# Kernel tuning notes

Hardware: AMD Instinct MI355X
Metric: run time of the kernel (lower is better)

The kernel has to match this reference:

```python
import jax, jax.numpy as jnp
import numpy as np

EPS = 1e-8


def _laplace_normalize(edge_row, edge_col, edge_vals, num_nodes):
    # D_r^{-1/2} A D_c^{-1/2} as in laplace_transform
    deg_r = jax.ops.segment_sum(edge_vals, edge_row, num_segments=num_nodes)
    deg_c = jax.ops.segment_sum(edge_vals, edge_col, num_segments=num_nodes)
    inv_r = 1.0 / (jnp.sqrt(deg_r) + EPS)
    inv_c = 1.0 / (jnp.sqrt(deg_c) + EPS)
    return edge_vals * inv_r[edge_row] * inv_c[edge_col]


def _l2norm(x):
    # F.normalize(p=2, dim=1): x / max(||x||, eps) with eps=1e-12
    n = jnp.sqrt(jnp.sum(x * x, axis=1, keepdims=True))
    return x / jnp.maximum(n, 1e-12)


def setup_inputs() -> dict:
    key = jax.random.key(0)
    k1, k2, k3, k4, k5, k6 = jax.random.split(key, 6)
    N, D, E, B = 100000, 64, 3200000, 4096
    node_features = jax.random.normal(k1, (N, D), dtype=jnp.float32)
    edge_row = jax.random.randint(k2, (E,), 0, N, dtype=jnp.int32)
    edge_col = jax.random.randint(k3, (E,), 0, N, dtype=jnp.int32)
    edge_vals = jnp.ones((E,), dtype=jnp.float32)
    a_id = jax.random.randint(k4, (B,), 0, N, dtype=jnp.int32)
    pos_id = jax.random.randint(k5, (B,), 0, N, dtype=jnp.int32)
    neg_id = jax.random.randint(k6, (B,), 0, N, dtype=jnp.int32)
    return {"node_features": node_features, "edge_row": edge_row,
            "edge_col": edge_col, "edge_vals": edge_vals,
            "a_id": a_id, "pos_id": pos_id, "neg_id": neg_id}


def reference(node_features, edge_row, edge_col, edge_vals, a_id, pos_id, neg_id):
    num_nodes = node_features.shape[0]
    num_layers = 3
    norm_vals = _laplace_normalize(edge_row, edge_col, edge_vals, num_nodes)

    # one_propagate: repeated spmm + per-layer L2 normalize, mean over layers
    features = node_features
    acc = node_features  # layer-0 term of the running sum (not normalized)
    for _ in range(num_layers):
        msgs = norm_vals[:, None] * features[edge_col]  # [E, D]
        features = jax.ops.segment_sum(msgs, edge_row, num_segments=num_nodes)
        acc = acc + _l2norm(features)
    node_rep = acc / (num_layers + 1)

    # BPR loss over batch
    a = node_rep[a_id]
    pos_pred = jnp.sum(a * node_rep[pos_id], axis=1)
    neg_pred = jnp.sum(a * node_rep[neg_id], axis=1)
    loss = jnp.mean(-jax.nn.log_sigmoid(pos_pred - neg_pred))
    return loss
```

## Files before the change

kernel.cpp:

```cpp
#include <hip/hip_runtime.h>
#include <math.h>

#define DDIM 64
#define BUCKET 1024
#define LRSHIFT 17
#define CMASK 0x1FFFF
#define LRMASK 0x3FF
#define NBLK 512
#define TPB_BIN 1024
#define NWV 16
#define TPB_CP 512
#define MAXNB 128

typedef unsigned long long ull;
typedef _Float16 half2_t __attribute__((ext_vector_type(2)));

__device__ inline unsigned int bf16_hi(float v) {
    unsigned int a = __float_as_uint(v);
    return (a + 0x7fffu + ((a >> 16) & 1u)) & 0xffff0000u;
}

__device__ inline unsigned int pk_f16x2(float lo, float hi) {
    return __builtin_bit_cast(unsigned int, __builtin_amdgcn_cvt_pkrtz(lo, hi));
}

__device__ inline half2_t dup_lo16(unsigned int s) {
    return __builtin_bit_cast(half2_t, __builtin_amdgcn_perm(0u, s, 0x01000100u));
}

__device__ inline half2_t h2_shfl_xor(half2_t v, int off) {
    return __builtin_bit_cast(half2_t, __shfl_xor(__builtin_bit_cast(unsigned int, v), off));
}

__global__ void init_fill_kernel(int* __restrict__ gfill_r, int* __restrict__ gfill_c,
                                 int NB, int cap) {
    int k = blockIdx.x * blockDim.x + threadIdx.x;
    if (k < NB) {
        gfill_r[k * 16] = k * cap;
        gfill_c[k * 16] = k * cap;
    }
}

__global__ __launch_bounds__(TPB_BIN)
void binning_kernel(const int* __restrict__ erow, const int* __restrict__ ecol,
                    const float* __restrict__ evals,
                    int* __restrict__ gfill_r, int* __restrict__ gfill_c,
                    ull* __restrict__ br, unsigned int* __restrict__ bc,
                    int E, int NB, int chunk) {
    __shared__ int hr[NWV][MAXNB];
    __shared__ int hc[NWV][MAXNB];
    __shared__ int fr[MAXNB];
    __shared__ int fc[MAXNB];
    int t = threadIdx.x;
    int wv = t >> 6;
    for (int k = t; k < NWV * MAXNB; k += TPB_BIN) { (&hr[0][0])[k] = 0; (&hc[0][0])[k] = 0; }
    __syncthreads();
    int lo = blockIdx.x * chunk;
    int hi = min(E, lo + chunk);
    int nq = (hi - lo) >> 2;
    int rem = (hi - lo) & 3;
    int p0 = t, p1 = t + TPB_BIN;
    bool h0 = p0 < nq, h1 = p1 < nq;
    int4 r40, c40, r41, c41;
    float4 v40, v41;
    if (h0) {
        int i = lo + 4 * p0;
        r40 = *(const int4*)(erow + i);
        c40 = *(const int4*)(ecol + i);
        v40 = *(const float4*)(evals + i);
        atomicAdd(&hr[wv][r40.x >> 10], 1);
        atomicAdd(&hr[wv][r40.y >> 10], 1);
        atomicAdd(&hr[wv][r40.z >> 10], 1);
        atomicAdd(&hr[wv][r40.w >> 10], 1);
        atomicAdd(&hc[wv][c40.x >> 10], 1);
        atomicAdd(&hc[wv][c40.y >> 10], 1);
        atomicAdd(&hc[wv][c40.z >> 10], 1);
        atomicAdd(&hc[wv][c40.w >> 10], 1);
    }
    if (h1) {
        int i = lo + 4 * p1;
        r41 = *(const int4*)(erow + i);
        c41 = *(const int4*)(ecol + i);
        v41 = *(const float4*)(evals + i);
        atomicAdd(&hr[wv][r41.x >> 10], 1);
        atomicAdd(&hr[wv][r41.y >> 10], 1);
        atomicAdd(&hr[wv][r41.z >> 10], 1);
        atomicAdd(&hr[wv][r41.w >> 10], 1);
        atomicAdd(&hc[wv][c41.x >> 10], 1);
        atomicAdd(&hc[wv][c41.y >> 10], 1);
        atomicAdd(&hc[wv][c41.z >> 10], 1);
        atomicAdd(&hc[wv][c41.w >> 10], 1);
    }
    if (t == 0) {
        for (int i = hi - rem; i < hi; i++) {
            atomicAdd(&hr[0][erow[i] >> 10], 1);
            atomicAdd(&hc[0][ecol[i] >> 10], 1);
        }
    }
    __syncthreads();
    if (t < NB) {
        int sr = 0, sc = 0;
        #pragma unroll
        for (int w2 = 0; w2 < NWV; w2++) { sr += hr[w2][t]; sc += hc[w2][t]; }
        fr[t] = atomicAdd(&gfill_r[t * 16], sr);
        fc[t] = atomicAdd(&gfill_c[t * 16], sc);
    }
    __syncthreads();
    if (h0) {
        int pos0 = atomicAdd(&fr[r40.x >> 10], 1);
        int pos1 = atomicAdd(&fr[r40.y >> 10], 1);
        int pos2 = atomicAdd(&fr[r40.z >> 10], 1);
        int pos3 = atomicAdd(&fr[r40.w >> 10], 1);
        br[pos0] = ((ull)__float_as_uint(v40.x) << 32) | ((ull)(r40.x & 1023) << LRSHIFT) | (unsigned)c40.x;
        br[pos1] = ((ull)__float_as_uint(v40.y) << 32) | ((ull)(r40.y & 1023) << LRSHIFT) | (unsigned)c40.y;
        br[pos2] = ((ull)__float_as_uint(v40.z) << 32) | ((ull)(r40.z & 1023) << LRSHIFT) | (unsigned)c40.z;
        br[pos3] = ((ull)__float_as_uint(v40.w) << 32) | ((ull)(r40.w & 1023) << LRSHIFT) | (unsigned)c40.w;
        int q0 = atomicAdd(&fc[c40.x >> 10], 1);
        int q1 = atomicAdd(&fc[c40.y >> 10], 1);
        int q2 = atomicAdd(&fc[c40.z >> 10], 1);
        int q3 = atomicAdd(&fc[c40.w >> 10], 1);
        bc[q0] = bf16_hi(v40.x) | (unsigned)(c40.x & 1023);
        bc[q1] = bf16_hi(v40.y) | (unsigned)(c40.y & 1023);
        bc[q2] = bf16_hi(v40.z) | (unsigned)(c40.z & 1023);
        bc[q3] = bf16_hi(v40.w) | (unsigned)(c40.w & 1023);
    }
    if (h1) {
        int pos0 = atomicAdd(&fr[r41.x >> 10], 1);
        int pos1 = atomicAdd(&fr[r41.y >> 10], 1);
        int pos2 = atomicAdd(&fr[r41.z >> 10], 1);
        int pos3 = atomicAdd(&fr[r41.w >> 10], 1);
        br[pos0] = ((ull)__float_as_uint(v41.x) << 32) | ((ull)(r41.x & 1023) << LRSHIFT) | (unsigned)c41.x;
        br[pos1] = ((ull)__float_as_uint(v41.y) << 32) | ((ull)(r41.y & 1023) << LRSHIFT) | (unsigned)c41.y;
        br[pos2] = ((ull)__float_as_uint(v41.z) << 32) | ((ull)(r41.z & 1023) << LRSHIFT) | (unsigned)c41.z;
        br[pos3] = ((ull)__float_as_uint(v41.w) << 32) | ((ull)(r41.w & 1023) << LRSHIFT) | (unsigned)c41.w;
        int q0 = atomicAdd(&fc[c41.x >> 10], 1);
        int q1 = atomicAdd(&fc[c41.y >> 10], 1);
        int q2 = atomicAdd(&fc[c41.z >> 10], 1);
        int q3 = atomicAdd(&fc[c41.w >> 10], 1);
        bc[q0] = bf16_hi(v41.x) | (unsigned)(c41.x & 1023);
        bc[q1] = bf16_hi(v41.y) | (unsigned)(c41.y & 1023);
        bc[q2] = bf16_hi(v41.z) | (unsigned)(c41.z & 1023);
        bc[q3] = bf16_hi(v41.w) | (unsigned)(c41.w & 1023);
    }
    if (t == 0) {
        for (int i = hi - rem; i < hi; i++) {
            int r = erow[i], c = ecol[i];
            float v = evals[i];
            int pos = atomicAdd(&fr[r >> 10], 1);
            br[pos] = ((ull)__float_as_uint(v) << 32) | ((ull)(r & 1023) << LRSHIFT) | (unsigned)c;
            int pos2 = atomicAdd(&fc[c >> 10], 1);
            bc[pos2] = bf16_hi(v) | (unsigned)(c & 1023);
        }
    }
}

__global__ __launch_bounds__(TPB_CP)
void count_kernel(const ull* __restrict__ br, const unsigned int* __restrict__ bc,
                  const int* __restrict__ gfill_r, const int* __restrict__ gfill_c,
                  int* __restrict__ subcnt, float* __restrict__ subds,
                  float* __restrict__ subdsc, int cap) {
    __shared__ int cnt[BUCKET];
    __shared__ float ds[BUCKET];
    __shared__ float dsc[BUCKET];
    int b = blockIdx.x >> 3, ch = blockIdx.x & 7;
    int t = threadIdx.x;
    for (int k = t; k < BUCKET; k += TPB_CP) { cnt[k] = 0; ds[k] = 0.0f; dsc[k] = 0.0f; }
    __syncthreads();
    int s = b * cap;
    int e = gfill_r[b * 16];
    int len = ((((e - s) + 7) >> 3) + 3) & ~3;
    int cs = s + ch * len, ce = min(e, cs + len);
    int m = cs + ((ce - cs) & ~3);
    for (int i = cs + 4 * t; i < m; i += 4 * TPB_CP) {
        ull p0 = br[i];
        ull p1 = br[i + 1];
        ull p2 = br[i + 2];
        ull p3 = br[i + 3];
        int lr0 = (int)((p0 >> LRSHIFT) & LRMASK);
        int lr1 = (int)((p1 >> LRSHIFT) & LRMASK);
        int lr2 = (int)((p2 >> LRSHIFT) & LRMASK);
        int lr3 = (int)((p3 >> LRSHIFT) & LRMASK);
        atomicAdd(&cnt[lr0], 1);
        atomicAdd(&cnt[lr1], 1);
        atomicAdd(&cnt[lr2], 1);
        atomicAdd(&cnt[lr3], 1);
        atomicAdd(&ds[lr0], __uint_as_float((unsigned)(p0 >> 32)));
        atomicAdd(&ds[lr1], __uint_as_float((unsigned)(p1 >> 32)));
        atomicAdd(&ds[lr2], __uint_as_float((unsigned)(p2 >> 32)));
        atomicAdd(&ds[lr3], __uint_as_float((unsigned)(p3 >> 32)));
    }
    if (t == 0) {
        for (int i = m; i < ce; i++) {
            ull p = br[i];
            int lr = (int)((p >> LRSHIFT) & LRMASK);
            atomicAdd(&cnt[lr], 1);
            atomicAdd(&ds[lr], __uint_as_float((unsigned)(p >> 32)));
        }
    }
    int e2 = gfill_c[b * 16];
    int len2 = ((((e2 - s) + 7) >> 3) + 3) & ~3;
    int cs2 = s + ch * len2, ce2 = min(e2, cs2 + len2);
    int m2 = cs2 + ((ce2 - cs2) & ~3);
    for (int i = cs2 + 4 * t; i < m2; i += 4 * TPB_CP) {
        uint4 p = *(const uint4*)(bc + i);
        atomicAdd(&dsc[p.x & 0x3FFu], __uint_as_float(p.x & 0xffff0000u));
        atomicAdd(&dsc[p.y & 0x3FFu], __uint_as_float(p.y & 0xffff0000u));
        atomicAdd(&dsc[p.z & 0x3FFu], __uint_as_float(p.z & 0xffff0000u));
        atomicAdd(&dsc[p.w & 0x3FFu], __uint_as_float(p.w & 0xffff0000u));
    }
    if (t == 0) {
        for (int i = m2; i < ce2; i++) {
            unsigned int p = bc[i];
            atomicAdd(&dsc[p & 0x3FFu], __uint_as_float(p & 0xffff0000u));
        }
    }
    __syncthreads();
    size_t base = ((size_t)b * 8 + ch) * BUCKET;
    for (int k = t; k < BUCKET; k += TPB_CP) {
        subcnt[base + k] = cnt[k];
        subds[base + k]  = ds[k];
        subdsc[base + k] = dsc[k];
    }
}

__global__ __launch_bounds__(1024)
void combine_kernel(int* __restrict__ subcnt, const float* __restrict__ subds,
                    const float* __restrict__ subdsc,
                    int2* __restrict__ rse,
                    float* __restrict__ inv_r, float* __restrict__ inv_c,
                    int N, int cap) {
    __shared__ int tot[BUCKET];
    int b = blockIdx.x, t = threadIdx.x;
    size_t base = (size_t)b * 8 * BUCKET;
    int c8[8];
    int sum = 0;
    #pragma unroll
    for (int c = 0; c < 8; c++) { c8[c] = subcnt[base + c * BUCKET + t]; sum += c8[c]; }
    int sum2 = (sum + 3) & ~3;
    tot[t] = sum2;
    __syncthreads();
    for (int off = 1; off < BUCKET; off <<= 1) {
        int v = (t >= off) ? tot[t - off] : 0;
        __syncthreads();
        tot[t] += v;
        __syncthreads();
    }
    int excl = tot[t] - sum2;
    int node = b * BUCKET + t;
    int s = b * cap;
    if (node < N) {
        int2 se;
        se.x = s + excl;
        se.y = s + excl + sum;
        rse[node] = se;
    }
    int run = s + excl;
    #pragma unroll
    for (int c = 0; c < 8; c++) { int v = c8[c]; subcnt[base + c * BUCKET + t] = run; run += v; }
    float d = 0.0f, dc = 0.0f;
    #pragma unroll
    for (int c = 0; c < 8; c++) { d += subds[base + c * BUCKET + t]; dc += subdsc[base + c * BUCKET + t]; }
    inv_r[b * BUCKET + t] = 1.0f / (sqrtf(d) + 1e-8f);
    inv_c[b * BUCKET + t] = 1.0f / (sqrtf(dc) + 1e-8f);
}

__global__ __launch_bounds__(TPB_CP)
void place_kernel(const ull* __restrict__ br, const int* __restrict__ gfill_r,
                  const int* __restrict__ pbase, const float* __restrict__ inv_r,
                  const float* __restrict__ inv_c,
                  unsigned int* __restrict__ cw, int cap) {
    __shared__ int fill[BUCKET];
    __shared__ float irs[BUCKET];
    int b = blockIdx.x >> 3, ch = blockIdx.x & 7;
    int t = threadIdx.x;
    size_t pb = ((size_t)b * 8 + ch) * BUCKET;
    for (int k = t; k < BUCKET; k += TPB_CP) {
        fill[k] = pbase[pb + k];
        irs[k]  = inv_r[b * BUCKET + k];
    }
    __syncthreads();
    int s = b * cap;
    int e = gfill_r[b * 16];
    int len = ((((e - s) + 7) >> 3) + 3) & ~3;
    int cs = s + ch * len, ce = min(e, cs + len);
    int m = cs + ((ce - cs) & ~3);
    for (int i = cs + 4 * t; i < m; i += 4 * TPB_CP) {
        ull p0 = br[i];
        ull p1 = br[i + 1];
        ull p2 = br[i + 2];
        ull p3 = br[i + 3];
        int c0 = (int)(p0 & CMASK), c1 = (int)(p1 & CMASK);
        int c2 = (int)(p2 & CMASK), c3 = (int)(p3 & CMASK);
        int lr0 = (int)((p0 >> LRSHIFT) & LRMASK);
        int lr1 = (int)((p1 >> LRSHIFT) & LRMASK);
        int lr2 = (int)((p2 >> LRSHIFT) & LRMASK);
        int lr3 = (int)((p3 >> LRSHIFT) & LRMASK);
        float v0 = __uint_as_float((unsigned)(p0 >> 32));
        float v1 = __uint_as_float((unsigned)(p1 >> 32));
        float v2 = __uint_as_float((unsigned)(p2 >> 32));
        float v3 = __uint_as_float((unsigned)(p3 >> 32));
        int pos0 = atomicAdd(&fill[lr0], 1);
        int pos1 = atomicAdd(&fill[lr1], 1);
        int pos2 = atomicAdd(&fill[lr2], 1);
        int pos3 = atomicAdd(&fill[lr3], 1);
        float w0 = v0 * inv_c[c0] * irs[lr0];
        float w1 = v1 * inv_c[c1] * irs[lr1];
        float w2 = v2 * inv_c[c2] * irs[lr2];
        float w3 = v3 * inv_c[c3] * irs[lr3];
        cw[pos0] = ((unsigned)c0 << 15) | ((pk_f16x2(w0, w0) & 0xFFFFu) >> 1);
        cw[pos1] = ((unsigned)c1 << 15) | ((pk_f16x2(w1, w1) & 0xFFFFu) >> 1);
        cw[pos2] = ((unsigned)c2 << 15) | ((pk_f16x2(w2, w2) & 0xFFFFu) >> 1);
        cw[pos3] = ((unsigned)c3 << 15) | ((pk_f16x2(w3, w3) & 0xFFFFu) >> 1);
    }
    if (t == 0) {
        for (int i = m; i < ce; i++) {
            ull p = br[i];
            int c = (int)(p & CMASK);
            int lr = (int)((p >> LRSHIFT) & LRMASK);
            float v = __uint_as_float((unsigned)(p >> 32));
            int pos = atomicAdd(&fill[lr], 1);
            float wv = v * inv_c[c] * irs[lr];
            cw[pos] = ((unsigned)c << 15) | ((pk_f16x2(wv, wv) & 0xFFFFu) >> 1);
        }
    }
}

__global__ void cvt_kernel(const float* __restrict__ src,
                           unsigned int* __restrict__ dst, long n4) {
    long i = (long)blockIdx.x * blockDim.x + threadIdx.x;
    if (i < n4) {
        float4 v = ((const float4*)src)[i];
        uint2 o;
        o.x = pk_f16x2(v.x, v.y);
        o.y = pk_f16x2(v.z, v.w);
        ((uint2*)dst)[i] = o;
    }
}

__global__ __launch_bounds__(256)
void spmm_f16_kernel(const int2* __restrict__ rse,
                     const unsigned int* __restrict__ cw,
                     const unsigned short* __restrict__ fin,
                     unsigned short* __restrict__ fout,
                     unsigned short* __restrict__ acc16, int N,
                     int writeOut, int initAcc) {
    int wid = blockIdx.x * (blockDim.x >> 6) + (threadIdx.x >> 6);
    if (wid >= N) return;
    int lane = threadIdx.x & 63;
    int g = lane >> 3;
    int h = lane & 7;
    int2 se = rse[wid];
    int s = se.x, e = se.y;
    uint4* ap = (uint4*)(acc16 + ((long)wid << 6)) + h;
    uint4 old = initAcc ? ((const uint4*)(fin + ((long)wid << 6)))[h] : *ap;
    half2_t a2[8];
    #pragma unroll
    for (int k = 0; k < 8; k++) a2[k] = (half2_t)0;

    for (int base = s; base < e; base += 32) {
        int j = base + 4 * g;
        if (j < e) {
            uint4 pw = *(const uint4*)(cw + j);
            int c0 = (int)(pw.x >> 15);
            int c1 = (j + 1 < e) ? (int)(pw.y >> 15) : c0;
            int c2 = (j + 2 < e) ? (int)(pw.z >> 15) : c0;
            int c3 = (j + 3 < e) ? (int)(pw.w >> 15) : c0;
            uint4 q0 = ((const uint4*)(fin + ((long)c0 << 6)))[h];
            uint4 q1 = ((const uint4*)(fin + ((long)c1 << 6)))[h];
            uint4 q2 = ((const uint4*)(fin + ((long)c2 << 6)))[h];
            uint4 q3 = ((const uint4*)(fin + ((long)c3 << 6)))[h];
            half2_t w0 = dup_lo16(pw.x << 1);
            half2_t w1 = (j + 1 < e) ? dup_lo16(pw.y << 1) : (half2_t)0;
            half2_t w2 = (j + 2 < e) ? dup_lo16(pw.z << 1) : (half2_t)0;
            half2_t w3 = (j + 3 < e) ? dup_lo16(pw.w << 1) : (half2_t)0;
            a2[0] += w0 * __builtin_bit_cast(half2_t, q0.x);
            a2[1] += w0 * __builtin_bit_cast(half2_t, q0.y);
            a2[2] += w0 * __builtin_bit_cast(half2_t, q0.z);
            a2[3] += w0 * __builtin_bit_cast(half2_t, q0.w);
            a2[4] += w1 * __builtin_bit_cast(half2_t, q1.x);
            a2[5] += w1 * __builtin_bit_cast(half2_t, q1.y);
            a2[6] += w1 * __builtin_bit_cast(half2_t, q1.z);
            a2[7] += w1 * __builtin_bit_cast(half2_t, q1.w);
            a2[0] += w2 * __builtin_bit_cast(half2_t, q2.x);
            a2[1] += w2 * __builtin_bit_cast(half2_t, q2.y);
            a2[2] += w2 * __builtin_bit_cast(half2_t, q2.z);
            a2[3] += w2 * __builtin_bit_cast(half2_t, q2.w);
            a2[4] += w3 * __builtin_bit_cast(half2_t, q3.x);
            a2[5] += w3 * __builtin_bit_cast(half2_t, q3.y);
            a2[6] += w3 * __builtin_bit_cast(half2_t, q3.z);
            a2[7] += w3 * __builtin_bit_cast(half2_t, q3.w);
        }
    }

    #pragma unroll
    for (int k = 0; k < 4; k++) a2[k] += a2[k + 4];
    #pragma unroll
    for (int k = 0; k < 4; k++) {
        a2[k] += h2_shfl_xor(a2[k], 8);
        a2[k] += h2_shfl_xor(a2[k], 16);
        a2[k] += h2_shfl_xor(a2[k], 32);
    }
    half2_t ssh = a2[0] * a2[0];
    ssh += a2[1] * a2[1];
    ssh += a2[2] * a2[2];
    ssh += a2[3] * a2[3];
    float ss = (float)ssh[0] + (float)ssh[1];
    ss += __shfl_xor(ss, 1);
    ss += __shfl_xor(ss, 2);
    ss += __shfl_xor(ss, 4);
    float s2 = fminf(1.0f / fmaxf(sqrtf(ss), 1e-12f), 6.0e4f);
    if (g == 0) {
        if (writeOut) {
            uint4 o;
            o.x = __builtin_bit_cast(unsigned int, a2[0]);
            o.y = __builtin_bit_cast(unsigned int, a2[1]);
            o.z = __builtin_bit_cast(unsigned int, a2[2]);
            o.w = __builtin_bit_cast(unsigned int, a2[3]);
            ((uint4*)(fout + ((long)wid << 6)))[h] = o;
        }
        half2_t s2h = __builtin_bit_cast(half2_t, pk_f16x2(s2, s2));
        uint4 nw;
        nw.x = __builtin_bit_cast(unsigned int, __builtin_bit_cast(half2_t, old.x) + a2[0] * s2h);
        nw.y = __builtin_bit_cast(unsigned int, __builtin_bit_cast(half2_t, old.y) + a2[1] * s2h);
        nw.z = __builtin_bit_cast(unsigned int, __builtin_bit_cast(half2_t, old.z) + a2[2] * s2h);
        nw.w = __builtin_bit_cast(unsigned int, __builtin_bit_cast(half2_t, old.w) + a2[3] * s2h);
        *ap = nw;
    }
}

__global__ void loss_terms_kernel(const unsigned short* __restrict__ acc16,
                                  const int* __restrict__ a_id, const int* __restrict__ p_id,
                                  const int* __restrict__ n_id,
                                  float* __restrict__ terms, int B) {
    long gid = (long)blockIdx.x * blockDim.x + threadIdx.x;
    int b = (int)(gid >> 6);
    int lane = threadIdx.x & 63;
    if (b < B) {
        int ia = a_id[b], ip = p_id[b], in2 = n_id[b];
        float a = (float)__builtin_bit_cast(_Float16, acc16[(long)ia * DDIM + lane]);
        float p = (float)__builtin_bit_cast(_Float16, acc16[(long)ip * DDIM + lane]);
        float n = (float)__builtin_bit_cast(_Float16, acc16[(long)in2 * DDIM + lane]);
        float dp = a * p, dn = a * n;
        #pragma unroll
        for (int off = 1; off < 64; off <<= 1) { dp += __shfl_xor(dp, off); dn += __shfl_xor(dn, off); }
        if (lane == 0) {
            float x = (dp - dn) * 0.0625f;
            terms[b] = fmaxf(-x, 0.0f) + log1pf(expf(-fabsf(x)));
        }
    }
}

__global__ void reduce_kernel(const float* __restrict__ terms, float* __restrict__ out, int B) {
    __shared__ float sm[256];
    float s = 0.0f;
    for (int i = threadIdx.x; i < B; i += 256) s += terms[i];
    sm[threadIdx.x] = s;
    __syncthreads();
    for (int stride = 128; stride > 0; stride >>= 1) {
        if (threadIdx.x < stride) sm[threadIdx.x] += sm[threadIdx.x + stride];
        __syncthreads();
    }
    if (threadIdx.x == 0) out[0] = sm[0] / (float)B;
}

extern "C" void kernel_launch(void* const* d_in, const int* in_sizes, int n_in,
                              void* d_out, int out_size, void* d_ws, size_t ws_size,
                              hipStream_t stream) {
    const float* nf    = (const float*)d_in[0];
    const int*   erow  = (const int*)d_in[1];
    const int*   ecol  = (const int*)d_in[2];
    const float* evals = (const float*)d_in[3];
    const int*   a_id  = (const int*)d_in[4];
    const int*   p_id  = (const int*)d_in[5];
    const int*   n_id  = (const int*)d_in[6];

    int N = in_sizes[0] / DDIM;
    int E = in_sizes[1];
    int B = in_sizes[4];
    int NB = (N + BUCKET - 1) / BUCKET;
    int chunk = (((E + NBLK - 1) / NBLK) + 3) & ~3;
    int Npad = NB * BUCKET;

    long capl = ((long)E * BUCKET) / N;
    int cap = (int)(capl + capl / 12 + 5120);
    cap = (cap + 63) & ~63;

    size_t regionA = (size_t)cap * NB * 8;
    size_t regionB = (size_t)cap * NB * 4;
    size_t featB16 = (size_t)N * DDIM * 2;
    if (regionA < 2 * featB16) regionA = 2 * featB16;
    size_t subBytes = (size_t)NB * 8 * BUCKET * 4;

    char* w = (char*)d_ws;
    ull*  br     = (ull*)w;
    char* regAp  = w;                 w += regionA;
    unsigned int* bc = (unsigned int*)w;
    unsigned int* cw = (unsigned int*)w;  w += regionB + 256;
    unsigned int* acc16 = (unsigned int*)w;  w += featB16;
    int* subcnt  = (int*)w;           w += subBytes;
    float* subds = (float*)w;         w += subBytes;
    float* subdsc= (float*)w;         w += subBytes;
    float* inv_c = (float*)w;         w += (size_t)Npad * 4;
    float* inv_r = (float*)w;         w += (size_t)Npad * 4;
    int2* rse    = (int2*)w;          w += (size_t)N * 8;
    int* gfill_r = (int*)w;           w += (size_t)NB * 16 * 4;
    int* gfill_c = (int*)w;           w += (size_t)NB * 16 * 4;
    float* terms = (float*)w;         w += (size_t)B * 4;

    unsigned short* fb0 = (unsigned short*)regAp;
    unsigned short* fb1 = (unsigned short*)(regAp + featB16);

    init_fill_kernel<<<1, 128, 0, stream>>>(gfill_r, gfill_c, NB, cap);
    binning_kernel<<<NBLK, TPB_BIN, 0, stream>>>(erow, ecol, evals, gfill_r, gfill_c,
                                                 br, bc, E, NB, chunk);
    count_kernel<<<NB * 8, TPB_CP, 0, stream>>>(br, bc, gfill_r, gfill_c,
                                                subcnt, subds, subdsc, cap);
    combine_kernel<<<NB, 1024, 0, stream>>>(subcnt, subds, subdsc, rse,
                                            inv_r, inv_c, N, cap);
    place_kernel<<<NB * 8, TPB_CP, 0, stream>>>(br, gfill_r, subcnt, inv_r, inv_c, cw, cap);

    long n4 = (long)N * DDIM / 4;
    cvt_kernel<<<(unsigned)((n4 + 255) / 256), 256, 0, stream>>>(nf, (unsigned int*)fb0, n4);

    unsigned spmmGrid = (unsigned)((N + 3) / 4);
    spmm_f16_kernel<<<spmmGrid, 256, 0, stream>>>(rse, cw, fb0, fb1,
                                                  (unsigned short*)acc16, N, 1, 1);
    spmm_f16_kernel<<<spmmGrid, 256, 0, stream>>>(rse, cw, fb1, fb0,
                                                  (unsigned short*)acc16, N, 1, 0);
    spmm_f16_kernel<<<spmmGrid, 256, 0, stream>>>(rse, cw, fb0, fb1,
                                                  (unsigned short*)acc16, N, 0, 0);

    loss_terms_kernel<<<(unsigned)(((long)B * 64 + 255) / 256), 256, 0, stream>>>(
        (const unsigned short*)acc16, a_id, p_id, n_id, terms, B);
    reduce_kernel<<<1, 256, 0, stream>>>(terms, (float*)d_out, B);
}
```

Measured before the change: 393.1 us.

## Replace bucketed binning CSR build with global-atomic histogram, scan and scatter

Replaces the two-level bucket binning (binning, count, combine, place kernels) with a direct CSR build: per-node global 64-bit atomics pack edge count and fixed-point degree sum, then a block scan plus a finalize pass compute row offsets, and a scatter kernel places edges using per-node atomic cursors. This removes the intermediate bucket buffers and one full pass over packed edges. In exchange it relies on millions of global atomics to random addresses, and it quantizes edge values to 16.16 fixed point for degree sums. The order of edges within a row becomes nondeterministic.

```diff
diff --git a/kernel.cpp b/kernel.cpp
--- a/kernel.cpp
+++ b/kernel.cpp
@@ -2,24 +2,14 @@
 #include <math.h>
 
 #define DDIM 64
-#define BUCKET 1024
-#define LRSHIFT 17
-#define CMASK 0x1FFFF
-#define LRMASK 0x3FF
-#define NBLK 512
-#define TPB_BIN 1024
-#define NWV 16
-#define TPB_CP 512
+#define SCANB 1024
 #define MAXNB 128
+#define FXBITS 40
+#define FXMASK 0xFFFFFFFFFFull
 
 typedef unsigned long long ull;
 typedef _Float16 half2_t __attribute__((ext_vector_type(2)));
 
-__device__ inline unsigned int bf16_hi(float v) {
-    unsigned int a = __float_as_uint(v);
-    return (a + 0x7fffu + ((a >> 16) & 1u)) & 0xffff0000u;
-}
-
 __device__ inline unsigned int pk_f16x2(float lo, float hi) {
     return __builtin_bit_cast(unsigned int, __builtin_amdgcn_cvt_pkrtz(lo, hi));
 }
@@ -32,295 +22,132 @@
     return __builtin_bit_cast(half2_t, __shfl_xor(__builtin_bit_cast(unsigned int, v), off));
 }
 
-__global__ void init_fill_kernel(int* __restrict__ gfill_r, int* __restrict__ gfill_c,
-                                 int NB, int cap) {
-    int k = blockIdx.x * blockDim.x + threadIdx.x;
-    if (k < NB) {
-        gfill_r[k * 16] = k * cap;
-        gfill_c[k * 16] = k * cap;
-    }
-}
-
-__global__ __launch_bounds__(TPB_BIN)
-void binning_kernel(const int* __restrict__ erow, const int* __restrict__ ecol,
-                    const float* __restrict__ evals,
-                    int* __restrict__ gfill_r, int* __restrict__ gfill_c,
-                    ull* __restrict__ br, unsigned int* __restrict__ bc,
-                    int E, int NB, int chunk) {
-    __shared__ int hr[NWV][MAXNB];
-    __shared__ int hc[NWV][MAXNB];
-    __shared__ int fr[MAXNB];
-    __shared__ int fc[MAXNB];
-    int t = threadIdx.x;
-    int wv = t >> 6;
-    for (int k = t; k < NWV * MAXNB; k += TPB_BIN) { (&hr[0][0])[k] = 0; (&hc[0][0])[k] = 0; }
+__device__ inline ull pack_edge(float v) {
+    return (1ull << FXBITS) | (ull)(unsigned)(int)(v * 65536.0f + 0.5f);
+}
+
+__global__ void zero_kernel(ull* __restrict__ p, long n) {
+    long i = (long)blockIdx.x * blockDim.x + threadIdx.x;
+    if (i < n) p[i] = 0;
+}
+
+__global__ __launch_bounds__(256)
+void hist_kernel(const int* __restrict__ erow, const int* __restrict__ ecol,
+                 const float* __restrict__ evals,
+                 ull* __restrict__ pr, ull* __restrict__ pc, int E) {
+    int nq = E >> 2;
+    for (int p = blockIdx.x * 256 + threadIdx.x; p < nq; p += gridDim.x * 256) {
+        int i = p << 2;
+        int4 r4 = *(const int4*)(erow + i);
+        int4 c4 = *(const int4*)(ecol + i);
+        float4 v4 = *(const float4*)(evals + i);
+        ull fx = pack_edge(v4.x);
+        ull fy = pack_edge(v4.y);
+        ull fz = pack_edge(v4.z);
+        ull fw = pack_edge(v4.w);
+        atomicAdd(&pr[r4.x], fx);
+        atomicAdd(&pr[r4.y], fy);
+        atomicAdd(&pr[r4.z], fz);
+        atomicAdd(&pr[r4.w], fw);
+        atomicAdd(&pc[c4.x], fx);
+        atomicAdd(&pc[c4.y], fy);
+        atomicAdd(&pc[c4.z], fz);
+        atomicAdd(&pc[c4.w], fw);
+    }
+    if (blockIdx.x == 0 && threadIdx.x == 0) {
+        for (int i = nq << 2; i < E; i++) {
+            ull f = pack_edge(evals[i]);
+            atomicAdd(&pr[erow[i]], f);
+            atomicAdd(&pc[ecol[i]], f);
+        }
+    }
+}
+
+__global__ __launch_bounds__(SCANB)
+void scan1_kernel(const ull* __restrict__ pr, const ull* __restrict__ pc,
+                  int* __restrict__ excl, int* __restrict__ btot,
+                  float* __restrict__ inv_r, float* __restrict__ inv_c) {
+    __shared__ int tot[SCANB];
+    int b = blockIdx.x, t = threadIdx.x;
+    int node = b * SCANB + t;
+    ull p = pr[node];
+    ull q = pc[node];
+    int cnt = (int)(p >> FXBITS);
+    float deg  = (float)((double)(p & FXMASK) * (1.0 / 65536.0));
+    float degc = (float)((double)(q & FXMASK) * (1.0 / 65536.0));
+    inv_r[node] = 1.0f / (sqrtf(deg)  + 1e-8f);
+    inv_c[node] = 1.0f / (sqrtf(degc) + 1e-8f);
+    int sum4 = (cnt + 3) & ~3;
+    tot[t] = sum4;
     __syncthreads();
-    int lo = blockIdx.x * chunk;
-    int hi = min(E, lo + chunk);
-    int nq = (hi - lo) >> 2;
-    int rem = (hi - lo) & 3;
-    int p0 = t, p1 = t + TPB_BIN;
-    bool h0 = p0 < nq, h1 = p1 < nq;
-    int4 r40, c40, r41, c41;
-    float4 v40, v41;
-    if (h0) {
-        int i = lo + 4 * p0;
-        r40 = *(const int4*)(erow + i);
-        c40 = *(const int4*)(ecol + i);
-        v40 = *(const float4*)(evals + i);
-        atomicAdd(&hr[wv][r40.x >> 10], 1);
-        atomicAdd(&hr[wv][r40.y >> 10], 1);
-        atomicAdd(&hr[wv][r40.z >> 10], 1);
-        atomicAdd(&hr[wv][r40.w >> 10], 1);
-        atomicAdd(&hc[wv][c40.x >> 10], 1);
-        atomicAdd(&hc[wv][c40.y >> 10], 1);
-        atomicAdd(&hc[wv][c40.z >> 10], 1);
-        atomicAdd(&hc[wv][c40.w >> 10], 1);
-    }
-    if (h1) {
-        int i = lo + 4 * p1;
-        r41 = *(const int4*)(erow + i);
-        c41 = *(const int4*)(ecol + i);
-        v41 = *(const float4*)(evals + i);
-        atomicAdd(&hr[wv][r41.x >> 10], 1);
-        atomicAdd(&hr[wv][r41.y >> 10], 1);
-        atomicAdd(&hr[wv][r41.z >> 10], 1);
-        atomicAdd(&hr[wv][r41.w >> 10], 1);
-        atomicAdd(&hc[wv][c41.x >> 10], 1);
-        atomicAdd(&hc[wv][c41.y >> 10], 1);
-        atomicAdd(&hc[wv][c41.z >> 10], 1);
-        atomicAdd(&hc[wv][c41.w >> 10], 1);
-    }
-    if (t == 0) {
-        for (int i = hi - rem; i < hi; i++) {
-            atomicAdd(&hr[0][erow[i] >> 10], 1);
-            atomicAdd(&hc[0][ecol[i] >> 10], 1);
-        }
-    }
+    for (int off = 1; off < SCANB; off <<= 1) {
+        int v = (t >= off) ? tot[t - off] : 0;
+        __syncthreads();
+        tot[t] += v;
+        __syncthreads();
+    }
+    excl[node] = tot[t] - sum4;
+    if (t == SCANB - 1) btot[b] = tot[t];
+}
+
+__global__ __launch_bounds__(SCANB)
+void finalize_kernel(const ull* __restrict__ pr, const int* __restrict__ excl,
+                     const int* __restrict__ btot,
+                     int2* __restrict__ rse, int* __restrict__ cur, int N, int NB) {
+    __shared__ int bo[MAXNB];
+    int b = blockIdx.x, t = threadIdx.x;
+    if (t < MAXNB) bo[t] = (t < NB) ? btot[t] : 0;
     __syncthreads();
-    if (t < NB) {
-        int sr = 0, sc = 0;
-        #pragma unroll
-        for (int w2 = 0; w2 < NWV; w2++) { sr += hr[w2][t]; sc += hc[w2][t]; }
-        fr[t] = atomicAdd(&gfill_r[t * 16], sr);
-        fc[t] = atomicAdd(&gfill_c[t * 16], sc);
-    }
-    __syncthreads();
-    if (h0) {
-        int pos0 = atomicAdd(&fr[r40.x >> 10], 1);
-        int pos1 = atomicAdd(&fr[r40.y >> 10], 1);
-        int pos2 = atomicAdd(&fr[r40.z >> 10], 1);
-        int pos3 = atomicAdd(&fr[r40.w >> 10], 1);
-        br[pos0] = ((ull)__float_as_uint(v40.x) << 32) | ((ull)(r40.x & 1023) << LRSHIFT) | (unsigned)c40.x;
-        br[pos1] = ((ull)__float_as_uint(v40.y) << 32) | ((ull)(r40.y & 1023) << LRSHIFT) | (unsigned)c40.y;
-        br[pos2] = ((ull)__float_as_uint(v40.z) << 32) | ((ull)(r40.z & 1023) << LRSHIFT) | (unsigned)c40.z;
-        br[pos3] = ((ull)__float_as_uint(v40.w) << 32) | ((ull)(r40.w & 1023) << LRSHIFT) | (unsigned)c40.w;
-        int q0 = atomicAdd(&fc[c40.x >> 10], 1);
-        int q1 = atomicAdd(&fc[c40.y >> 10], 1);
-        int q2 = atomicAdd(&fc[c40.z >> 10], 1);
-        int q3 = atomicAdd(&fc[c40.w >> 10], 1);
-        bc[q0] = bf16_hi(v40.x) | (unsigned)(c40.x & 1023);
-        bc[q1] = bf16_hi(v40.y) | (unsigned)(c40.y & 1023);
-        bc[q2] = bf16_hi(v40.z) | (unsigned)(c40.z & 1023);
-        bc[q3] = bf16_hi(v40.w) | (unsigned)(c40.w & 1023);
-    }
-    if (h1) {
-        int pos0 = atomicAdd(&fr[r41.x >> 10], 1);
-        int pos1 = atomicAdd(&fr[r41.y >> 10], 1);
-        int pos2 = atomicAdd(&fr[r41.z >> 10], 1);
-        int pos3 = atomicAdd(&fr[r41.w >> 10], 1);
-        br[pos0] = ((ull)__float_as_uint(v41.x) << 32) | ((ull)(r41.x & 1023) << LRSHIFT) | (unsigned)c41.x;
-        br[pos1] = ((ull)__float_as_uint(v41.y) << 32) | ((ull)(r41.y & 1023) << LRSHIFT) | (unsigned)c41.y;
-        br[pos2] = ((ull)__float_as_uint(v41.z) << 32) | ((ull)(r41.z & 1023) << LRSHIFT) | (unsigned)c41.z;
-        br[pos3] = ((ull)__float_as_uint(v41.w) << 32) | ((ull)(r41.w & 1023) << LRSHIFT) | (unsigned)c41.w;
-        int q0 = atomicAdd(&fc[c41.x >> 10], 1);
-        int q1 = atomicAdd(&fc[c41.y >> 10], 1);
-        int q2 = atomicAdd(&fc[c41.z >> 10], 1);
-        int q3 = atomicAdd(&fc[c41.w >> 10], 1);
-        bc[q0] = bf16_hi(v41.x) | (unsigned)(c41.x & 1023);
-        bc[q1] = bf16_hi(v41.y) | (unsigned)(c41.y & 1023);
-        bc[q2] = bf16_hi(v41.z) | (unsigned)(c41.z & 1023);
-        bc[q3] = bf16_hi(v41.w) | (unsigned)(c41.w & 1023);
-    }
-    if (t == 0) {
-        for (int i = hi - rem; i < hi; i++) {
-            int r = erow[i], c = ecol[i];
-            float v = evals[i];
-            int pos = atomicAdd(&fr[r >> 10], 1);
-            br[pos] = ((ull)__float_as_uint(v) << 32) | ((ull)(r & 1023) << LRSHIFT) | (unsigned)c;
-            int pos2 = atomicAdd(&fc[c >> 10], 1);
-            bc[pos2] = bf16_hi(v) | (unsigned)(c & 1023);
-        }
-    }
-}
-
-__global__ __launch_bounds__(TPB_CP)
-void count_kernel(const ull* __restrict__ br, const unsigned int* __restrict__ bc,
-                  const int* __restrict__ gfill_r, const int* __restrict__ gfill_c,
-                  int* __restrict__ subcnt, float* __restrict__ subds,
-                  float* __restrict__ subdsc, int cap) {
-    __shared__ int cnt[BUCKET];
-    __shared__ float ds[BUCKET];
-    __shared__ float dsc[BUCKET];
-    int b = blockIdx.x >> 3, ch = blockIdx.x & 7;
-    int t = threadIdx.x;
-    for (int k = t; k < BUCKET; k += TPB_CP) { cnt[k] = 0; ds[k] = 0.0f; dsc[k] = 0.0f; }
-    __syncthreads();
-    int s = b * cap;
-    int e = gfill_r[b * 16];
-    int len = ((((e - s) + 7) >> 3) + 3) & ~3;
-    int cs = s + ch * len, ce = min(e, cs + len);
-    int m = cs + ((ce - cs) & ~3);
-    for (int i = cs + 4 * t; i < m; i += 4 * TPB_CP) {
-        ull p0 = br[i];
-        ull p1 = br[i + 1];
-        ull p2 = br[i + 2];
-        ull p3 = br[i + 3];
-        int lr0 = (int)((p0 >> LRSHIFT) & LRMASK);
-        int lr1 = (int)((p1 >> LRSHIFT) & LRMASK);
-        int lr2 = (int)((p2 >> LRSHIFT) & LRMASK);
-        int lr3 = (int)((p3 >> LRSHIFT) & LRMASK);
-        atomicAdd(&cnt[lr0], 1);
-        atomicAdd(&cnt[lr1], 1);
-        atomicAdd(&cnt[lr2], 1);
-        atomicAdd(&cnt[lr3], 1);
-        atomicAdd(&ds[lr0], __uint_as_float((unsigned)(p0 >> 32)));
-        atomicAdd(&ds[lr1], __uint_as_float((unsigned)(p1 >> 32)));
-        atomicAdd(&ds[lr2], __uint_as_float((unsigned)(p2 >> 32)));
-        atomicAdd(&ds[lr3], __uint_as_float((unsigned)(p3 >> 32)));
-    }
-    if (t == 0) {
-        for (int i = m; i < ce; i++) {
-            ull p = br[i];
-            int lr = (int)((p >> LRSHIFT) & LRMASK);
-            atomicAdd(&cnt[lr], 1);
-            atomicAdd(&ds[lr], __uint_as_float((unsigned)(p >> 32)));
-        }
-    }
-    int e2 = gfill_c[b * 16];
-    int len2 = ((((e2 - s) + 7) >> 3) + 3) & ~3;
-    int cs2 = s + ch * len2, ce2 = min(e2, cs2 + len2);
-    int m2 = cs2 + ((ce2 - cs2) & ~3);
-    for (int i = cs2 + 4 * t; i < m2; i += 4 * TPB_CP) {
-        uint4 p = *(const uint4*)(bc + i);
-        atomicAdd(&dsc[p.x & 0x3FFu], __uint_as_float(p.x & 0xffff0000u));
-        atomicAdd(&dsc[p.y & 0x3FFu], __uint_as_float(p.y & 0xffff0000u));
-        atomicAdd(&dsc[p.z & 0x3FFu], __uint_as_float(p.z & 0xffff0000u));
-        atomicAdd(&dsc[p.w & 0x3FFu], __uint_as_float(p.w & 0xffff0000u));
-    }
-    if (t == 0) {
-        for (int i = m2; i < ce2; i++) {
-            unsigned int p = bc[i];
-            atomicAdd(&dsc[p & 0x3FFu], __uint_as_float(p & 0xffff0000u));
-        }
-    }
-    __syncthreads();
-    size_t base = ((size_t)b * 8 + ch) * BUCKET;
-    for (int k = t; k < BUCKET; k += TPB_CP) {
-        subcnt[base + k] = cnt[k];
-        subds[base + k]  = ds[k];
-        subdsc[base + k] = dsc[k];
-    }
-}
-
-__global__ __launch_bounds__(1024)
-void combine_kernel(int* __restrict__ subcnt, const float* __restrict__ subds,
-                    const float* __restrict__ subdsc,
-                    int2* __restrict__ rse,
-                    float* __restrict__ inv_r, float* __restrict__ inv_c,
-                    int N, int cap) {
-    __shared__ int tot[BUCKET];
-    int b = blockIdx.x, t = threadIdx.x;
-    size_t base = (size_t)b * 8 * BUCKET;
-    int c8[8];
-    int sum = 0;
-    #pragma unroll
-    for (int c = 0; c < 8; c++) { c8[c] = subcnt[base + c * BUCKET + t]; sum += c8[c]; }
-    int sum2 = (sum + 3) & ~3;
-    tot[t] = sum2;
-    __syncthreads();
-    for (int off = 1; off < BUCKET; off <<= 1) {
-        int v = (t >= off) ? tot[t - off] : 0;
-        __syncthreads();
-        tot[t] += v;
-        __syncthreads();
-    }
-    int excl = tot[t] - sum2;
-    int node = b * BUCKET + t;
-    int s = b * cap;
+    for (int off = 1; off < MAXNB; off <<= 1) {
+        int v = 0;
+        if (t >= off && t < MAXNB) v = bo[t - off];
+        __syncthreads();
+        if (t < MAXNB) bo[t] += v;
+        __syncthreads();
+    }
+    int base = (b == 0) ? 0 : bo[b - 1];
+    int node = b * SCANB + t;
+    int cnt = (int)(pr[node] >> FXBITS);
+    int st = base + excl[node];
     if (node < N) {
         int2 se;
-        se.x = s + excl;
-        se.y = s + excl + sum;
+        se.x = st;
+        se.y = st + cnt;
         rse[node] = se;
     }
-    int run = s + excl;
-    #pragma unroll
-    for (int c = 0; c < 8; c++) { int v = c8[c]; subcnt[base + c * BUCKET + t] = run; run += v; }
-    float d = 0.0f, dc = 0.0f;
-    #pragma unroll
-    for (int c = 0; c < 8; c++) { d += subds[base + c * BUCKET + t]; dc += subdsc[base + c * BUCKET + t]; }
-    inv_r[b * BUCKET + t] = 1.0f / (sqrtf(d) + 1e-8f);
-    inv_c[b * BUCKET + t] = 1.0f / (sqrtf(dc) + 1e-8f);
-}
-
-__global__ __launch_bounds__(TPB_CP)
-void place_kernel(const ull* __restrict__ br, const int* __restrict__ gfill_r,
-                  const int* __restrict__ pbase, const float* __restrict__ inv_r,
-                  const float* __restrict__ inv_c,
-                  unsigned int* __restrict__ cw, int cap) {
-    __shared__ int fill[BUCKET];
-    __shared__ float irs[BUCKET];
-    int b = blockIdx.x >> 3, ch = blockIdx.x & 7;
-    int t = threadIdx.x;
-    size_t pb = ((size_t)b * 8 + ch) * BUCKET;
-    for (int k = t; k < BUCKET; k += TPB_CP) {
-        fill[k] = pbase[pb + k];
-        irs[k]  = inv_r[b * BUCKET + k];
-    }
-    __syncthreads();
-    int s = b * cap;
-    int e = gfill_r[b * 16];
-    int len = ((((e - s) + 7) >> 3) + 3) & ~3;
-    int cs = s + ch * len, ce = min(e, cs + len);
-    int m = cs + ((ce - cs) & ~3);
-    for (int i = cs + 4 * t; i < m; i += 4 * TPB_CP) {
-        ull p0 = br[i];
-        ull p1 = br[i + 1];
-        ull p2 = br[i + 2];
-        ull p3 = br[i + 3];
-        int c0 = (int)(p0 & CMASK), c1 = (int)(p1 & CMASK);
-        int c2 = (int)(p2 & CMASK), c3 = (int)(p3 & CMASK);
-        int lr0 = (int)((p0 >> LRSHIFT) & LRMASK);
-        int lr1 = (int)((p1 >> LRSHIFT) & LRMASK);
-        int lr2 = (int)((p2 >> LRSHIFT) & LRMASK);
-        int lr3 = (int)((p3 >> LRSHIFT) & LRMASK);
-        float v0 = __uint_as_float((unsigned)(p0 >> 32));
-        float v1 = __uint_as_float((unsigned)(p1 >> 32));
-        float v2 = __uint_as_float((unsigned)(p2 >> 32));
-        float v3 = __uint_as_float((unsigned)(p3 >> 32));
-        int pos0 = atomicAdd(&fill[lr0], 1);
-        int pos1 = atomicAdd(&fill[lr1], 1);
-        int pos2 = atomicAdd(&fill[lr2], 1);
-        int pos3 = atomicAdd(&fill[lr3], 1);
-        float w0 = v0 * inv_c[c0] * irs[lr0];
-        float w1 = v1 * inv_c[c1] * irs[lr1];
-        float w2 = v2 * inv_c[c2] * irs[lr2];
-        float w3 = v3 * inv_c[c3] * irs[lr3];
-        cw[pos0] = ((unsigned)c0 << 15) | ((pk_f16x2(w0, w0) & 0xFFFFu) >> 1);
-        cw[pos1] = ((unsigned)c1 << 15) | ((pk_f16x2(w1, w1) & 0xFFFFu) >> 1);
-        cw[pos2] = ((unsigned)c2 << 15) | ((pk_f16x2(w2, w2) & 0xFFFFu) >> 1);
-        cw[pos3] = ((unsigned)c3 << 15) | ((pk_f16x2(w3, w3) & 0xFFFFu) >> 1);
-    }
-    if (t == 0) {
-        for (int i = m; i < ce; i++) {
-            ull p = br[i];
-            int c = (int)(p & CMASK);
-            int lr = (int)((p >> LRSHIFT) & LRMASK);
-            float v = __uint_as_float((unsigned)(p >> 32));
-            int pos = atomicAdd(&fill[lr], 1);
-            float wv = v * inv_c[c] * irs[lr];
-            cw[pos] = ((unsigned)c << 15) | ((pk_f16x2(wv, wv) & 0xFFFFu) >> 1);
+    cur[node] = st;
+}
+
+__global__ __launch_bounds__(256)
+void place2_kernel(const int* __restrict__ erow, const int* __restrict__ ecol,
+                   const float* __restrict__ evals,
+                   const float* __restrict__ inv_r, const float* __restrict__ inv_c,
+                   int* __restrict__ cur, unsigned int* __restrict__ cw, int E) {
+    int nq = E >> 2;
+    for (int p = blockIdx.x * 256 + threadIdx.x; p < nq; p += gridDim.x * 256) {
+        int i = p << 2;
+        int4 r4 = *(const int4*)(erow + i);
+        int4 c4 = *(const int4*)(ecol + i);
+        float4 v4 = *(const float4*)(evals + i);
+        int pos0 = atomicAdd(&cur[r4.x], 1);
+        int pos1 = atomicAdd(&cur[r4.y], 1);
+        int pos2 = atomicAdd(&cur[r4.z], 1);
+        int pos3 = atomicAdd(&cur[r4.w], 1);
+        float w0 = v4.x * inv_r[r4.x] * inv_c[c4.x];
+        float w1 = v4.y * inv_r[r4.y] * inv_c[c4.y];
+        float w2 = v4.z * inv_r[r4.z] * inv_c[c4.z];
+        float w3 = v4.w * inv_r[r4.w] * inv_c[c4.w];
+        cw[pos0] = ((unsigned)c4.x << 15) | ((pk_f16x2(w0, w0) & 0xFFFFu) >> 1);
+        cw[pos1] = ((unsigned)c4.y << 15) | ((pk_f16x2(w1, w1) & 0xFFFFu) >> 1);
+        cw[pos2] = ((unsigned)c4.z << 15) | ((pk_f16x2(w2, w2) & 0xFFFFu) >> 1);
+        cw[pos3] = ((unsigned)c4.w << 15) | ((pk_f16x2(w3, w3) & 0xFFFFu) >> 1);
+    }
+    if (blockIdx.x == 0 && threadIdx.x == 0) {
+        for (int i = nq << 2; i < E; i++) {
+            int r = erow[i], c = ecol[i];
+            int pos = atomicAdd(&cur[r], 1);
+            float w = evals[i] * inv_r[r] * inv_c[c];
+            cw[pos] = ((unsigned)c << 15) | ((pk_f16x2(w, w) & 0xFFFFu) >> 1);
         }
     }
 }
@@ -477,47 +304,33 @@
     int N = in_sizes[0] / DDIM;
     int E = in_sizes[1];
     int B = in_sizes[4];
-    int NB = (N + BUCKET - 1) / BUCKET;
-    int chunk = (((E + NBLK - 1) / NBLK) + 3) & ~3;
-    int Npad = NB * BUCKET;
-
-    long capl = ((long)E * BUCKET) / N;
-    int cap = (int)(capl + capl / 12 + 5120);
-    cap = (cap + 63) & ~63;
-
-    size_t regionA = (size_t)cap * NB * 8;
-    size_t regionB = (size_t)cap * NB * 4;
+    int NB = (N + SCANB - 1) / SCANB;
+    int Npad = NB * SCANB;
+
     size_t featB16 = (size_t)N * DDIM * 2;
-    if (regionA < 2 * featB16) regionA = 2 * featB16;
-    size_t subBytes = (size_t)NB * 8 * BUCKET * 4;
+    size_t cwWords = (size_t)E + 3 * (size_t)N + 256;
 
     char* w = (char*)d_ws;
-    ull*  br     = (ull*)w;
-    char* regAp  = w;                 w += regionA;
-    unsigned int* bc = (unsigned int*)w;
-    unsigned int* cw = (unsigned int*)w;  w += regionB + 256;
-    unsigned int* acc16 = (unsigned int*)w;  w += featB16;
-    int* subcnt  = (int*)w;           w += subBytes;
-    float* subds = (float*)w;         w += subBytes;
-    float* subdsc= (float*)w;         w += subBytes;
-    float* inv_c = (float*)w;         w += (size_t)Npad * 4;
-    float* inv_r = (float*)w;         w += (size_t)Npad * 4;
-    int2* rse    = (int2*)w;          w += (size_t)N * 8;
-    int* gfill_r = (int*)w;           w += (size_t)NB * 16 * 4;
-    int* gfill_c = (int*)w;           w += (size_t)NB * 16 * 4;
-    float* terms = (float*)w;         w += (size_t)B * 4;
-
-    unsigned short* fb0 = (unsigned short*)regAp;
-    unsigned short* fb1 = (unsigned short*)(regAp + featB16);
-
-    init_fill_kernel<<<1, 128, 0, stream>>>(gfill_r, gfill_c, NB, cap);
-    binning_kernel<<<NBLK, TPB_BIN, 0, stream>>>(erow, ecol, evals, gfill_r, gfill_c,
-                                                 br, bc, E, NB, chunk);
-    count_kernel<<<NB * 8, TPB_CP, 0, stream>>>(br, bc, gfill_r, gfill_c,
-                                                subcnt, subds, subdsc, cap);
-    combine_kernel<<<NB, 1024, 0, stream>>>(subcnt, subds, subdsc, rse,
-                                            inv_r, inv_c, N, cap);
-    place_kernel<<<NB * 8, TPB_CP, 0, stream>>>(br, gfill_r, subcnt, inv_r, inv_c, cw, cap);
+    unsigned short* fb0 = (unsigned short*)w;  w += (featB16 + 255) & ~(size_t)255;
+    unsigned short* fb1 = (unsigned short*)w;  w += (featB16 + 255) & ~(size_t)255;
+    unsigned short* acc16 = (unsigned short*)w; w += (featB16 + 255) & ~(size_t)255;
+    unsigned int* cw = (unsigned int*)w;       w += (cwWords * 4 + 255) & ~(size_t)255;
+    ull* packed_r = (ull*)w;                   w += (size_t)Npad * 8;
+    ull* packed_c = (ull*)w;                   w += (size_t)Npad * 8;
+    float* inv_r = (float*)w;                  w += (size_t)Npad * 4;
+    float* inv_c = (float*)w;                  w += (size_t)Npad * 4;
+    int* excl = (int*)w;                       w += (size_t)Npad * 4;
+    int* cur = (int*)w;                        w += (size_t)Npad * 4;
+    int* btot = (int*)w;                       w += (size_t)MAXNB * 4;
+    int2* rse = (int2*)w;                      w += (size_t)N * 8;
+    float* terms = (float*)w;                  w += (size_t)B * 4;
+
+    long nzero = 2L * Npad;
+    zero_kernel<<<(unsigned)((nzero + 255) / 256), 256, 0, stream>>>(packed_r, nzero);
+    hist_kernel<<<1024, 256, 0, stream>>>(erow, ecol, evals, packed_r, packed_c, E);
+    scan1_kernel<<<NB, SCANB, 0, stream>>>(packed_r, packed_c, excl, btot, inv_r, inv_c);
+    finalize_kernel<<<NB, SCANB, 0, stream>>>(packed_r, excl, btot, rse, cur, N, NB);
+    place2_kernel<<<1024, 256, 0, stream>>>(erow, ecol, evals, inv_r, inv_c, cur, cw, E);
 
     long n4 = (long)N * DDIM / 4;
     cvt_kernel<<<(unsigned)((n4 + 255) / 256), 256, 0, stream>>>(nf, (unsigned int*)fb0, n4);
```

New measurement: 750.8 us. 1.91x slower.

## Compute layer normalization and accumulation only for batch nodes in loss kernel

Applied to the files above, without the earlier changes.

The per-node accumulator update and per-layer L2 normalization are removed from the SpMM kernel, which now only writes layer outputs into three separate f16 buffers. The loss kernel rebuilds node representations on demand for the sampled anchor, positive and negative ids by gathering the original features and the three layer outputs and normalizing each. This avoids reading and writing the full N x D accumulator in every SpMM pass and skips normalization for nodes the loss never uses. In exchange it needs a third feature buffer and does more gathers and reductions per batch row in the loss kernel.

```diff
diff --git a/kernel.cpp b/kernel.cpp
--- a/kernel.cpp
+++ b/kernel.cpp
@@ -341,9 +341,7 @@
 void spmm_f16_kernel(const int2* __restrict__ rse,
                      const unsigned int* __restrict__ cw,
                      const unsigned short* __restrict__ fin,
-                     unsigned short* __restrict__ fout,
-                     unsigned short* __restrict__ acc16, int N,
-                     int writeOut, int initAcc) {
+                     unsigned short* __restrict__ fout, int N) {
     int wid = blockIdx.x * (blockDim.x >> 6) + (threadIdx.x >> 6);
     if (wid >= N) return;
     int lane = threadIdx.x & 63;
@@ -351,8 +349,6 @@
     int h = lane & 7;
     int2 se = rse[wid];
     int s = se.x, e = se.y;
-    uint4* ap = (uint4*)(acc16 + ((long)wid << 6)) + h;
-    uint4 old = initAcc ? ((const uint4*)(fin + ((long)wid << 6)))[h] : *ap;
     half2_t a2[8];
     #pragma unroll
     for (int k = 0; k < 8; k++) a2[k] = (half2_t)0;
@@ -400,35 +396,43 @@
         a2[k] += h2_shfl_xor(a2[k], 16);
         a2[k] += h2_shfl_xor(a2[k], 32);
     }
-    half2_t ssh = a2[0] * a2[0];
-    ssh += a2[1] * a2[1];
-    ssh += a2[2] * a2[2];
-    ssh += a2[3] * a2[3];
-    float ss = (float)ssh[0] + (float)ssh[1];
-    ss += __shfl_xor(ss, 1);
-    ss += __shfl_xor(ss, 2);
-    ss += __shfl_xor(ss, 4);
-    float s2 = fminf(1.0f / fmaxf(sqrtf(ss), 1e-12f), 6.0e4f);
     if (g == 0) {
-        if (writeOut) {
-            uint4 o;
-            o.x = __builtin_bit_cast(unsigned int, a2[0]);
-            o.y = __builtin_bit_cast(unsigned int, a2[1]);
-            o.z = __builtin_bit_cast(unsigned int, a2[2]);
-            o.w = __builtin_bit_cast(unsigned int, a2[3]);
-            ((uint4*)(fout + ((long)wid << 6)))[h] = o;
-        }
-        half2_t s2h = __builtin_bit_cast(half2_t, pk_f16x2(s2, s2));
-        uint4 nw;
-        nw.x = __builtin_bit_cast(unsigned int, __builtin_bit_cast(half2_t, old.x) + a2[0] * s2h);
-        nw.y = __builtin_bit_cast(unsigned int, __builtin_bit_cast(half2_t, old.y) + a2[1] * s2h);
-        nw.z = __builtin_bit_cast(unsigned int, __builtin_bit_cast(half2_t, old.z) + a2[2] * s2h);
-        nw.w = __builtin_bit_cast(unsigned int, __builtin_bit_cast(half2_t, old.w) + a2[3] * s2h);
-        *ap = nw;
-    }
-}
-
-__global__ void loss_terms_kernel(const unsigned short* __restrict__ acc16,
+        uint4 o;
+        o.x = __builtin_bit_cast(unsigned int, a2[0]);
+        o.y = __builtin_bit_cast(unsigned int, a2[1]);
+        o.z = __builtin_bit_cast(unsigned int, a2[2]);
+        o.w = __builtin_bit_cast(unsigned int, a2[3]);
+        ((uint4*)(fout + ((long)wid << 6)))[h] = o;
+    }
+}
+
+__device__ inline float rep_at(const float* __restrict__ nf,
+                               const unsigned short* __restrict__ f1,
+                               const unsigned short* __restrict__ f2,
+                               const unsigned short* __restrict__ f3,
+                               int id, int lane) {
+    long off = (long)id * DDIM + lane;
+    float r  = nf[off];
+    float v1 = (float)__builtin_bit_cast(_Float16, f1[off]);
+    float v2 = (float)__builtin_bit_cast(_Float16, f2[off]);
+    float v3 = (float)__builtin_bit_cast(_Float16, f3[off]);
+    float s1 = v1 * v1, s2 = v2 * v2, s3 = v3 * v3;
+    #pragma unroll
+    for (int o = 1; o < 64; o <<= 1) {
+        s1 += __shfl_xor(s1, o);
+        s2 += __shfl_xor(s2, o);
+        s3 += __shfl_xor(s3, o);
+    }
+    r += v1 / fmaxf(sqrtf(s1), 1e-12f);
+    r += v2 / fmaxf(sqrtf(s2), 1e-12f);
+    r += v3 / fmaxf(sqrtf(s3), 1e-12f);
+    return r;
+}
+
+__global__ void loss_terms_kernel(const float* __restrict__ nf,
+                                  const unsigned short* __restrict__ f1,
+                                  const unsigned short* __restrict__ f2,
+                                  const unsigned short* __restrict__ f3,
                                   const int* __restrict__ a_id, const int* __restrict__ p_id,
                                   const int* __restrict__ n_id,
                                   float* __restrict__ terms, int B) {
@@ -436,11 +440,10 @@
     int b = (int)(gid >> 6);
     int lane = threadIdx.x & 63;
     if (b < B) {
-        int ia = a_id[b], ip = p_id[b], in2 = n_id[b];
-        float a = (float)__builtin_bit_cast(_Float16, acc16[(long)ia * DDIM + lane]);
-        float p = (float)__builtin_bit_cast(_Float16, acc16[(long)ip * DDIM + lane]);
-        float n = (float)__builtin_bit_cast(_Float16, acc16[(long)in2 * DDIM + lane]);
-        float dp = a * p, dn = a * n;
+        float ra = rep_at(nf, f1, f2, f3, a_id[b], lane);
+        float rp = rep_at(nf, f1, f2, f3, p_id[b], lane);
+        float rn = rep_at(nf, f1, f2, f3, n_id[b], lane);
+        float dp = ra * rp, dn = ra * rn;
         #pragma unroll
         for (int off = 1; off < 64; off <<= 1) { dp += __shfl_xor(dp, off); dn += __shfl_xor(dn, off); }
         if (lane == 0) {
@@ -496,7 +499,7 @@
     char* regAp  = w;                 w += regionA;
     unsigned int* bc = (unsigned int*)w;
     unsigned int* cw = (unsigned int*)w;  w += regionB + 256;
-    unsigned int* acc16 = (unsigned int*)w;  w += featB16;
+    unsigned short* fb2 = (unsigned short*)w;  w += featB16;
     int* subcnt  = (int*)w;           w += subBytes;
     float* subds = (float*)w;         w += subBytes;
     float* subdsc= (float*)w;         w += subBytes;
@@ -523,14 +526,11 @@
     cvt_kernel<<<(unsigned)((n4 + 255) / 256), 256, 0, stream>>>(nf, (unsigned int*)fb0, n4);
 
     unsigned spmmGrid = (unsigned)((N + 3) / 4);
-    spmm_f16_kernel<<<spmmGrid, 256, 0, stream>>>(rse, cw, fb0, fb1,
-                                                  (unsigned short*)acc16, N, 1, 1);
-    spmm_f16_kernel<<<spmmGrid, 256, 0, stream>>>(rse, cw, fb1, fb0,
-                                                  (unsigned short*)acc16, N, 1, 0);
-    spmm_f16_kernel<<<spmmGrid, 256, 0, stream>>>(rse, cw, fb0, fb1,
-                                                  (unsigned short*)acc16, N, 0, 0);
+    spmm_f16_kernel<<<spmmGrid, 256, 0, stream>>>(rse, cw, fb0, fb1, N);
+    spmm_f16_kernel<<<spmmGrid, 256, 0, stream>>>(rse, cw, fb1, fb2, N);
+    spmm_f16_kernel<<<spmmGrid, 256, 0, stream>>>(rse, cw, fb2, fb0, N);
 
     loss_terms_kernel<<<(unsigned)(((long)B * 64 + 255) / 256), 256, 0, stream>>>(
-        (const unsigned short*)acc16, a_id, p_id, n_id, terms, B);
+        nf, fb1, fb2, fb0, a_id, p_id, n_id, terms, B);
     reduce_kernel<<<1, 256, 0, stream>>>(terms, (float*)d_out, B);
 }
```

Result: faster. 382.5 us (-2.7%).
